# Kernel optimization log

Hardware: AMD Instinct MI355X
Metric: run time of the kernel (lower is better)

The kernel has to match this reference:

```python
import jax, jax.numpy as jnp
import numpy as np

B, T, DIM = 4, 2048, 2048
H = 16
Q_LORA, KV_LORA = 1536, 512
ROPE_D, NOPE_D, V_D = 64, 128, 128
Q_HEAD_D = NOPE_D + ROPE_D  # 192
EPS = 1e-6
ROPE_THETA = 500000.0


def rmsnorm(x, w):
    xf = x.astype(jnp.float32)
    rms = jax.lax.rsqrt(jnp.mean(xf * xf, axis=-1, keepdims=True) + EPS)
    return (xf * rms).astype(x.dtype) * w


def apply_rope(x, cos, sin):
    # x: (B,T,H,d); cos/sin: (T,d//2). Complex mult on interleaved pairs.
    d = x.shape[-1]
    xp = x.reshape(*x.shape[:-1], d // 2, 2)
    x0, x1 = xp[..., 0], xp[..., 1]
    c = cos[None, :, None, :]
    s = sin[None, :, None, :]
    o0 = x0 * c - x1 * s
    o1 = x0 * s + x1 * c
    return jnp.stack([o0, o1], axis=-1).reshape(x.shape)


def setup_inputs() -> dict:
    key = jax.random.key(0)
    ks = jax.random.split(key, 8)
    x = jax.random.normal(ks[0], (B, T, DIM), dtype=jnp.float32)
    # RoPE freqs as in standard precompute_freqs_cis
    inv_freq = 1.0 / (ROPE_THETA ** (np.arange(0, ROPE_D, 2, dtype=np.float32) / ROPE_D))
    t = np.arange(T, dtype=np.float32)
    ang = np.outer(t, inv_freq)  # (T, 32)
    freqs_cos = jnp.asarray(np.cos(ang))
    freqs_sin = jnp.asarray(np.sin(ang))
    # causal additive mask (1,1,T,T)
    mask = jnp.where(jnp.tril(jnp.ones((T, T), dtype=bool)), 0.0, -1e9).astype(jnp.float32)[None, None]
    sc = lambda fan_in: 1.0 / np.sqrt(fan_in)
    q_down_w = jax.random.normal(ks[1], (Q_LORA, DIM), dtype=jnp.float32) * sc(DIM)
    q_norm_w = jnp.ones((Q_LORA,), dtype=jnp.float32)
    q_up_nope_w = jax.random.normal(ks[2], (H * NOPE_D, Q_LORA), dtype=jnp.float32) * sc(Q_LORA)
    q_up_rope_w = jax.random.normal(ks[3], (H * ROPE_D, Q_LORA), dtype=jnp.float32) * sc(Q_LORA)
    kv_down_w = jax.random.normal(ks[4], (KV_LORA + ROPE_D, DIM), dtype=jnp.float32) * sc(DIM)
    kv_norm_w = jnp.ones((KV_LORA,), dtype=jnp.float32)
    kv_up_w = jax.random.normal(ks[5], (H * (NOPE_D + V_D), KV_LORA), dtype=jnp.float32) * sc(KV_LORA)
    wo_w = jax.random.normal(ks[6], (DIM, H * V_D), dtype=jnp.float32) * sc(H * V_D)
    return {"x": x, "freqs_cos": freqs_cos, "freqs_sin": freqs_sin, "mask": mask,
            "q_down_w": q_down_w, "q_norm_w": q_norm_w, "q_up_nope_w": q_up_nope_w,
            "q_up_rope_w": q_up_rope_w, "kv_down_w": kv_down_w, "kv_norm_w": kv_norm_w,
            "kv_up_w": kv_up_w, "wo_w": wo_w}


def reference(x, freqs_cos, freqs_sin, mask, q_down_w, q_norm_w, q_up_nope_w,
              q_up_rope_w, kv_down_w, kv_norm_w, kv_up_w, wo_w):
    b, t, _ = x.shape
    # Q path: low-rank down -> RMSNorm -> nope/rope up projections
    c_q = rmsnorm(x @ q_down_w.T, q_norm_w)                      # (B,T,q_lora)
    q_nope = (c_q @ q_up_nope_w.T).reshape(b, t, H, NOPE_D)
    q_rope = (c_q @ q_up_rope_w.T).reshape(b, t, H, ROPE_D)
    q_rope = apply_rope(q_rope, freqs_cos, freqs_sin)
    q = jnp.concatenate([q_nope, q_rope], axis=-1)               # (B,T,H,192)
    # KV path: shared low-rank latent + per-sequence rope key
    kv_raw = x @ kv_down_w.T                                     # (B,T,512+64)
    c_kv = kv_raw[..., :KV_LORA]
    k_rope = kv_raw[..., KV_LORA:][:, :, None, :]                # (B,T,1,64)
    k_rope = apply_rope(k_rope, freqs_cos, freqs_sin)
    k_rope = jnp.broadcast_to(k_rope, (b, t, H, ROPE_D))
    kv = (rmsnorm(c_kv, kv_norm_w) @ kv_up_w.T).reshape(b, t, H, NOPE_D + V_D)
    k_nope = kv[..., :NOPE_D]
    v = kv[..., NOPE_D:]                                         # (B,T,H,128)
    k = jnp.concatenate([k_nope, k_rope], axis=-1)               # (B,T,H,192)
    scale = Q_HEAD_D ** -0.5
    attn = jnp.einsum('bthd,bshd->bhts', q, k) * scale + mask    # (B,H,T,T)
    attn = jax.nn.softmax(attn, axis=-1)
    out = jnp.einsum('bhts,bshd->bthd', attn, v).reshape(b, t, H * V_D)
    return out @ wo_w.T
```

## Files before the change

kernel.cpp:

```cpp
#include <hip/hip_runtime.h>

#define BB 4
#define TT 2048
#define HH 16
#define ROWS (BB*TT)

typedef unsigned short u16;
typedef __bf16 bf16x8 __attribute__((ext_vector_type(8)));
typedef float f32x4 __attribute__((ext_vector_type(4)));
typedef u16 u16x8 __attribute__((ext_vector_type(8)));
typedef u16 u16x4 __attribute__((ext_vector_type(4)));

__device__ __forceinline__ u16 f2bf(float f) {
  unsigned u = __float_as_uint(f);
  u += 0x7fffu + ((u >> 16) & 1u);
  return (u16)(u >> 16);
}
__device__ __forceinline__ float bf2f(u16 h) {
  return __uint_as_float(((unsigned)h) << 16);
}

__device__ __forceinline__ void gload_lds16(const u16* g, u16* l) {
  __builtin_amdgcn_global_load_lds((const __attribute__((address_space(1))) void*)g,
                                   (__attribute__((address_space(3))) void*)l, 16, 0, 0);
}

__global__ __launch_bounds__(256) void cast_all(const float* __restrict__ x,
                                                const float* __restrict__ qdw,
                                                const float* __restrict__ kvdw,
                                                const float* __restrict__ qunw,
                                                const float* __restrict__ qurw,
                                                const float* __restrict__ kvuw,
                                                const float* __restrict__ wow,
                                                u16* __restrict__ xb,
                                                u16* __restrict__ wdc,
                                                u16* __restrict__ wuc,
                                                u16* __restrict__ wkvu,
                                                u16* __restrict__ wwo,
                                                float qsc) {
  const long s0 = 1536L*2048, s1 = 768L*2048, s2 = 2048L*1536,
             s3 = 1024L*1536, s4 = 4096L*512,  s5 = 2048L*2048,
             s6 = (long)ROWS*2048;
  const long total = s0+s1+s2+s3+s4+s5+s6;
  long i = ((long)blockIdx.x * 256 + threadIdx.x) * 4;
  long stride = (long)gridDim.x * 1024;
  for (; i < total; i += stride) {
    long off = i; const float* src; u16* dst; float sc = 1.f; long lim = -1;
    if (off < s0)               { src = qdw;  dst = wdc; }
    else if ((off -= s0) < s1)  { src = kvdw; dst = wdc + s0; lim = 576L*2048; }
    else if ((off -= s1) < s2)  { src = qunw; dst = wuc; sc = qsc; }
    else if ((off -= s2) < s3)  { src = qurw; dst = wuc + s2; }
    else if ((off -= s3) < s4)  { src = kvuw; dst = wkvu; }
    else if ((off -= s4) < s5)  { src = wow;  dst = wwo; }
    else { off -= s5;             src = x;    dst = xb; }
    u16x4 o;
    if (lim < 0 || off + 3 < lim) {
      float4 v = *(const float4*)(src + off);
      o = (u16x4){ f2bf(v.x*sc), f2bf(v.y*sc), f2bf(v.z*sc), f2bf(v.w*sc) };
    } else {
#pragma unroll
      for (int e = 0; e < 4; ++e) o[e] = (off + e < lim) ? f2bf(src[off+e]*sc) : (u16)0;
    }
    *(u16x4*)(dst + off) = o;
  }
}

template<int MODE>
__global__ __launch_bounds__(512, 2) void gemm256(const u16* __restrict__ A,
                                                  const u16* __restrict__ Bm,
                                                  void* __restrict__ Cv,
                                                  u16* __restrict__ Vt,
                                                  int M, int N, int K, int lda) {
  __shared__ __align__(16) u16 lds[32768];
  const int tid = threadIdx.x;
  const int lane = tid & 63, wid = tid >> 6;
  const int wm = (wid >> 2) * 128;
  const int wn = (wid & 3) * 64;

  const int nx = gridDim.x;
  int id = blockIdx.y * nx + blockIdx.x;
  const int cpx = (nx * gridDim.y) >> 3;
  id = (id & 7) * cpx + (id >> 3);
  const int m0 = (id / nx) * 256;
  const int n0 = (id % nx) * 256;

  const int NT = K >> 5;

  f32x4 acc[8][4] = {};

  auto stage = [&](int kt, int d) {
#pragma unroll
    for (int j = 0; j < 2; ++j) {
      int c = j*512 + tid;
      int row = c >> 2;
      int colb = (c & 3) << 4;
      int srcb = colb ^ (((row >> 1) & 3) << 4);
      const u16* ga = (const u16*)((const char*)A + ((long)(m0 + row) * lda + kt*32) * 2 + srcb);
      gload_lds16(ga, (u16*)((char*)lds + d*32768 + c*16));
      const u16* gb = (const u16*)((const char*)Bm + ((long)(n0 + row) * K + kt*32) * 2 + srcb);
      gload_lds16(gb, (u16*)((char*)lds + d*32768 + 16384 + c*16));
    }
  };

  stage(0, 0);
  stage(1, 1);

  const int lr = lane & 15;
  const int kb = (lane >> 4) << 4;

  for (int kt = 0; kt < NT; ++kt) {
    const int cur = kt & 1;
    if (kt + 1 < NT) asm volatile("s_waitcnt vmcnt(4)" ::: "memory");
    else             asm volatile("s_waitcnt vmcnt(0)" ::: "memory");
    __builtin_amdgcn_s_barrier();
    __builtin_amdgcn_sched_barrier(0);

    const char* Ab = (const char*)lds + cur*32768;
    const char* Bb = Ab + 16384;
    bf16x8 af[8], bf[4];
#pragma unroll
    for (int i = 0; i < 8; ++i) {
      int r = wm + i*16 + lr;
      af[i] = *(const bf16x8*)(Ab + r*64 + (kb ^ (((r >> 1) & 3) << 4)));
    }
#pragma unroll
    for (int i = 0; i < 4; ++i) {
      int r = wn + i*16 + lr;
      bf[i] = *(const bf16x8*)(Bb + r*64 + (kb ^ (((r >> 1) & 3) << 4)));
    }
    __builtin_amdgcn_s_setprio(1);
#pragma unroll
    for (int i = 0; i < 8; ++i)
#pragma unroll
      for (int j = 0; j < 4; ++j)
        acc[i][j] = __builtin_amdgcn_mfma_f32_16x16x32_bf16(af[i], bf[j], acc[i][j], 0, 0, 0);
    __builtin_amdgcn_s_setprio(0);
    __builtin_amdgcn_sched_barrier(0);
    __builtin_amdgcn_s_barrier();
    if (kt + 2 < NT) stage(kt + 2, cur);
  }

  const int orow = (lane >> 4) << 2;
  const int ocol = lane & 15;
#pragma unroll
  for (int mf = 0; mf < 8; ++mf)
#pragma unroll
    for (int nf = 0; nf < 4; ++nf) {
      long rbase = (long)(m0 + wm + mf*16 + orow);
      int col = n0 + wn + nf*16 + ocol;
      if (MODE == 0) {
#pragma unroll
        for (int rr = 0; rr < 4; ++rr)
          ((float*)Cv)[(rbase + rr) * (long)N + col] = acc[mf][nf][rr];
      } else if (MODE == 1) {
#pragma unroll
        for (int rr = 0; rr < 4; ++rr)
          ((u16*)Cv)[(rbase + rr) * (long)N + col] = f2bf(acc[mf][nf][rr]);
      } else {
        int h = col >> 8, inner = col & 255;
        if (inner < 128) {
#pragma unroll
          for (int rr = 0; rr < 4; ++rr)
            ((u16*)Cv)[(rbase + rr) * 2048L + h*128 + inner] = f2bf(acc[mf][nf][rr]);
        } else {
          int bb = (int)(rbase >> 11);
          int t  = (int)(rbase & 2047);
          long vo = ((long)(bb*16 + h) * 128 + (inner - 128)) * 2048 + t;
          u16x4 o = { f2bf(acc[mf][nf][0]), f2bf(acc[mf][nf][1]),
                      f2bf(acc[mf][nf][2]), f2bf(acc[mf][nf][3]) };
          *(u16x4*)(Vt + vo) = o;
        }
      }
    }
}

__global__ __launch_bounds__(256) void rms_rope_dk(u16* __restrict__ dk,
                                                   const float* __restrict__ qnw,
                                                   const float* __restrict__ kvnw,
                                                   u16* __restrict__ Kr,
                                                   const float* __restrict__ cosb,
                                                   const float* __restrict__ sinb) {
  const long row = blockIdx.x;
  u16* x = dk + row * 2304;
  const int i = threadIdx.x * 8;
  float sq = 0.f, sk = 0.f;
  u16x8 v = *(const u16x8*)(x + i);
  {
    float s = 0.f;
#pragma unroll
    for (int e = 0; e < 8; ++e) { float f = bf2f(v[e]); s += f*f; }
    if (i < 1536) sq = s; else sk = s;
  }
#pragma unroll
  for (int off = 32; off > 0; off >>= 1) {
    sq += __shfl_down(sq, off);
    sk += __shfl_down(sk, off);
  }
  __shared__ float redq[4], redk[4];
  if ((threadIdx.x & 63) == 0) {
    redq[threadIdx.x >> 6] = sq;
    redk[threadIdx.x >> 6] = sk;
  }
  __syncthreads();
  float rq = rsqrtf((redq[0]+redq[1]+redq[2]+redq[3]) * (1.f/1536.f) + 1e-6f);
  float rk = rsqrtf((redk[0]+redk[1]+redk[2]+redk[3]) * (1.f/512.f) + 1e-6f);
  {
    float r = (i < 1536) ? rq : rk;
    const float* w = (i < 1536) ? (qnw + i) : (kvnw + (i - 1536));
    u16x8 o;
#pragma unroll
    for (int e = 0; e < 8; ++e) o[e] = f2bf(bf2f(v[e]) * r * w[e]);
    *(u16x8*)(x + i) = o;
  }
  if (threadIdx.x < 32) {
    const int t = (int)(row & (TT-1));
    int ii = threadIdx.x;
    float x0 = bf2f(x[2048 + 2*ii]);
    float x1 = bf2f(x[2048 + 2*ii + 1]);
    float c = cosb[t*32 + ii], s = sinb[t*32 + ii];
    Kr[row*64 + 2*ii]     = f2bf(x0*c - x1*s);
    Kr[row*64 + 2*ii + 1] = f2bf(x0*s + x1*c);
  }
}

__global__ __launch_bounds__(512) void flash_attn10(const u16* __restrict__ qcat,
                                                    const u16* __restrict__ kn,
                                                    const u16* __restrict__ kr,
                                                    const u16* __restrict__ Vt,
                                                    const float* __restrict__ cosb,
                                                    const float* __restrict__ sinb,
                                                    u16* __restrict__ O) {
  __shared__ __align__(16) u16 lds[36864];
  const int bid = blockIdx.x;
  const int u = bid & 255, sl = bid >> 8;
  const int a = u >> 6;
  const int bh = u & 63;
  const int qt = sl ? a : (7 - a);
  const int b = bh >> 4, h = bh & 15;
  const int wid = threadIdx.x >> 6, lane = threadIdx.x & 63;
  const int q0 = qt*256 + wid*32;
  const long browq = (long)b * TT + q0;
  const long browk = (long)b * TT;
  const int l16 = lane >> 4;
  const int l8  = lane >> 3;
  const int lx16   = (lane & 15) * 16;
  const int lx8_16 = (lane & 7) * 16;
  const int co = l16 * 16;
  const float QSCE = 0.10411754661f;

  bf16x8 qf[2][6];
#pragma unroll
  for (int f = 0; f < 2; ++f) {
    long row = browq + f*16 + (lane & 15);
#pragma unroll
    for (int ks = 0; ks < 4; ++ks)
      qf[f][ks] = *(const bf16x8*)(qcat + row * 3072 + h*128 + ks*32 + l16 * 8);
    const int t = (int)(row & (TT-1));
#pragma unroll
    for (int ks = 0; ks < 2; ++ks) {
      bf16x8 v = *(const bf16x8*)(qcat + row * 3072 + 2048 + h*64 + ks*32 + l16 * 8);
      const int ib = ks*16 + l16*4;
#pragma unroll
      for (int pp = 0; pp < 4; ++pp) {
        float x0 = (float)v[2*pp], x1 = (float)v[2*pp+1];
        float c = cosb[t*32 + ib + pp], s = sinb[t*32 + ib + pp];
        v[2*pp]   = (__bf16)((x0*c - x1*s) * QSCE);
        v[2*pp+1] = (__bf16)((x0*s + x1*c) * QSCE);
      }
      qf[f][4+ks] = v;
    }
  }

  bf16x8 vones;
#pragma unroll
  for (int e = 0; e < 8; ++e) vones[e] = (__bf16)1.0f;

  f32x4 oacc[2][8] = {};
  f32x4 lsum[2] = {};

  u16* pw = lds + 20480 + wid * 2048;

  const int nIter = 4*qt + 4;
  for (int it = 0; it < nIter; ++it) {
    const int s0 = it * 64;
#pragma unroll
    for (int j = 0; j < 2; ++j) {
      int c = j*8 + wid;
      int r = c*4 + l16;
      int cb = lx16 ^ ((r & 7) << 4);
      const u16* src = (const u16*)((const char*)kn + (browk + s0 + r) * 4096 + h * 256 + cb);
      gload_lds16(src, lds + c*512);
    }
    {
      int c = wid;
      int r = c*8 + l8;
      int cb = lx8_16 ^ ((r & 7) << 4);
      const u16* src = (const u16*)((const char*)kr + (browk + s0 + r) * 128 + cb);
      gload_lds16(src, lds + 8192 + c*512);
    }
#pragma unroll
    for (int j = 0; j < 2; ++j) {
      int c = j*8 + wid;
      int d = c*8 + l8;
      int cb = lx8_16 ^ ((d & 7) << 4);
      const u16* src = (const u16*)((const char*)Vt + ((long)bh*128 + d) * (TT*2) + (long)s0*2 + cb);
      gload_lds16(src, lds + 12288 + c*512);
    }
    __syncthreads();

    const bool skip0 = s0 > q0 + 15;
    const bool skip1 = s0 > q0 + 31;
    if (!skip0 || !skip1) {
      __builtin_amdgcn_s_setprio(1);
      f32x4 sacc[2][4] = {};
#pragma unroll
      for (int nt = 0; nt < 4; ++nt) {
        const int r = nt*16 + (lane & 15);
        const int swz = (r & 7) << 4;
        bf16x8 kf[6];
#pragma unroll
        for (int ks = 0; ks < 4; ++ks)
          kf[ks] = *(const bf16x8*)((const char*)lds + r*256 + ((ks*64 + co) ^ swz));
#pragma unroll
        for (int ks = 0; ks < 2; ++ks)
          kf[4+ks] = *(const bf16x8*)((const char*)lds + 16384 + r*128 + ((ks*64 + co) ^ swz));
        if (!skip0) {
#pragma unroll
          for (int ks = 0; ks < 6; ++ks)
            sacc[0][nt] = __builtin_amdgcn_mfma_f32_16x16x32_bf16(qf[0][ks], kf[ks], sacc[0][nt], 0, 0, 0);
        }
        if (!skip1) {
#pragma unroll
          for (int ks = 0; ks < 6; ++ks)
            sacc[1][nt] = __builtin_amdgcn_mfma_f32_16x16x32_bf16(qf[1][ks], kf[ks], sacc[1][nt], 0, 0, 0);
        }
      }
#pragma unroll
      for (int f = 0; f < 2; ++f) {
        const bool skipf = f ? skip1 : skip0;
        if (skipf) continue;
        const int qmin = q0 + f*16;
        const int qb = qmin + (l16 << 2);
        if (s0 + 63 > qmin) {
#pragma unroll
          for (int nt = 0; nt < 4; ++nt) {
            int sc = s0 + nt*16 + (lane & 15);
#pragma unroll
            for (int rr = 0; rr < 4; ++rr)
              if (sc > qb + rr) sacc[f][nt][rr] = -1e30f;
          }
        }
        const int lb2 = (lane & 15) * 2;
#pragma unroll
        for (int rr = 0; rr < 4; ++rr) {
          float p0 = exp2f(sacc[f][0][rr] - 16.f);
          float p1 = exp2f(sacc[f][1][rr] - 16.f);
          float p2 = exp2f(sacc[f][2][rr] - 16.f);
          float p3 = exp2f(sacc[f][3][rr] - 16.f);
          const int prow = f*16 + (l16 << 2) + rr;
          const int sw = (prow & 7) << 4;
          char* pb = (char*)pw + prow*128;
          *(u16*)(pb + ((     lb2) ^ sw)) = f2bf(p0);
          *(u16*)(pb + (( 32 + lb2) ^ sw)) = f2bf(p1);
          *(u16*)(pb + (( 64 + lb2) ^ sw)) = f2bf(p2);
          *(u16*)(pb + (( 96 + lb2) ^ sw)) = f2bf(p3);
        }
      }
#pragma unroll
      for (int ks = 0; ks < 2; ++ks) {
        const int cb = ks*64 + co;
        bf16x8 vf[8];
#pragma unroll
        for (int vt = 0; vt < 8; ++vt) {
          int row = vt*16 + (lane & 15);
          vf[vt] = *(const bf16x8*)((const char*)lds + 24576 + row*128 + (cb ^ ((row & 7) << 4)));
        }
#pragma unroll
        for (int f = 0; f < 2; ++f) {
          if (f ? skip1 : skip0) continue;
          int prow = f*16 + (lane & 15);
          bf16x8 pa = *(const bf16x8*)((const char*)pw + prow*128 + (cb ^ ((prow & 7) << 4)));
          lsum[f] = __builtin_amdgcn_mfma_f32_16x16x32_bf16(pa, vones, lsum[f], 0, 0, 0);
#pragma unroll
          for (int vt = 0; vt < 8; ++vt)
            oacc[f][vt] = __builtin_amdgcn_mfma_f32_16x16x32_bf16(pa, vf[vt], oacc[f][vt], 0, 0, 0);
        }
      }
      __builtin_amdgcn_s_setprio(0);
    }
    __syncthreads();
  }

#pragma unroll
  for (int f = 0; f < 2; ++f) {
    float inv[4];
#pragma unroll
    for (int rr = 0; rr < 4; ++rr) inv[rr] = 1.f / lsum[f][rr];
#pragma unroll
    for (int vt = 0; vt < 8; ++vt)
#pragma unroll
      for (int rr = 0; rr < 4; ++rr) {
        long row = browq + f*16 + (l16 << 2) + rr;
        int col = h*128 + vt*16 + (lane & 15);
        O[row * 2048 + col] = f2bf(oacc[f][vt][rr] * inv[rr]);
      }
  }
}

static inline long minl(long a, long b) { return a < b ? a : b; }

extern "C" void kernel_launch(void* const* d_in, const int* in_sizes, int n_in,
                              void* d_out, int out_size, void* d_ws, size_t ws_size,
                              hipStream_t stream) {
  const float* x    = (const float*)d_in[0];
  const float* fcos = (const float*)d_in[1];
  const float* fsin = (const float*)d_in[2];
  const float* qdw  = (const float*)d_in[4];
  const float* qnw  = (const float*)d_in[5];
  const float* qunw = (const float*)d_in[6];
  const float* qurw = (const float*)d_in[7];
  const float* kvdw = (const float*)d_in[8];
  const float* kvnw = (const float*)d_in[9];
  const float* kvuw = (const float*)d_in[10];
  const float* wow  = (const float*)d_in[11];
  float* out = (float*)d_out;

  char* p = (char*)d_ws;
  auto alloc = [&](size_t bytes) { char* r = p; p += (bytes + 255) & ~(size_t)255; return r; };

  u16* xb   = (u16*)alloc((size_t)ROWS*2048*2);
  u16* wdc  = (u16*)alloc((size_t)2304*2048*2);
  u16* wuc  = (u16*)alloc((size_t)3072*1536*2);
  u16* wkvu = (u16*)alloc((size_t)4096*512*2);
  u16* wwo  = (u16*)alloc((size_t)2048*2048*2);
  u16* dk   = (u16*)alloc((size_t)ROWS*2304*2);
  u16* qcat = (u16*)alloc((size_t)ROWS*3072*2);
  u16* kn   = (u16*)alloc((size_t)ROWS*2048*2);
  u16* Vt   = (u16*)alloc((size_t)ROWS*2048*2);
  u16* kro  = (u16*)alloc((size_t)ROWS*64*2);

  u16* Ob = xb;

  const float QSC_E = 0.10411754661f;

  cast_all<<<4096, 256, 0, stream>>>(x, qdw, kvdw, qunw, qurw, kvuw, wow,
                                     xb, wdc, wuc, wkvu, wwo, QSC_E);

  gemm256<1><<<dim3(9, 32), 512, 0, stream>>>(xb, wdc, dk, nullptr, ROWS, 2304, 2048, 2048);
  rms_rope_dk<<<ROWS, 256, 0, stream>>>(dk, qnw, kvnw, kro, fcos, fsin);
  gemm256<1><<<dim3(12, 32), 512, 0, stream>>>(dk, wuc, qcat, nullptr, ROWS, 3072, 1536, 2304);
  gemm256<2><<<dim3(16, 32), 512, 0, stream>>>(dk + 1536, wkvu, kn, Vt, ROWS, 4096, 512, 2304);
  flash_attn10<<<512, 512, 0, stream>>>(qcat, kn, kro, Vt, fcos, fsin, Ob);
  gemm256<0><<<dim3(8, 32), 512, 0, stream>>>(Ob, wwo, out, nullptr, ROWS, 2048, 2048, 2048);
}
```

Before: 538.6 us.

## Add split-K-half pipelined GEMM variant for kv_up and output projection

Introduces gemm256k, a 256x256 tile GEMM that stages each 64-wide K tile as two 32-wide halves in double-buffered LDS. It issues next-tile loads interleaved between MFMA groups, using partial vmcnt waits and s_setprio around the MFMAs. It also remaps block IDs into 8 groups to improve L2 locality. The kv_up and wo GEMMs switch to this kernel, aiming to overlap global-to-LDS traffic with compute; the finer-grained barriers add synchronization cost.

```diff
diff --git a/kernel.cpp b/kernel.cpp
--- a/kernel.cpp
+++ b/kernel.cpp
@@ -174,6 +174,125 @@
     }
 }
 
+template<int MODE>
+__global__ __launch_bounds__(512, 2) void gemm256k(const u16* __restrict__ A,
+                                                   const u16* __restrict__ Bm,
+                                                   void* __restrict__ Cv,
+                                                   u16* __restrict__ Vt,
+                                                   int M, int N, int K, int lda) {
+  __shared__ __align__(16) u16 lds[65536];
+  const int tid = threadIdx.x;
+  const int lane = tid & 63, wid = tid >> 6;
+  const int wm = (wid >> 2) * 128;
+  const int wn = (wid & 3) * 64;
+
+  const int nx = gridDim.x;
+  int id = blockIdx.y * nx + blockIdx.x;
+  const int cpx = (nx * gridDim.y) >> 3;
+  id = (id & 7) * cpx + (id >> 3);
+  const int m0 = (id / nx) * 256;
+  const int n0 = (id % nx) * 256;
+
+  const int NT = K >> 6;
+
+  f32x4 acc[8][4] = {};
+
+  auto stageH = [&](int mat, int j, int t) {
+    const int d = t & 1;
+    char* base = (char*)lds + mat*65536 + (j*2 + d)*16384;
+    const u16* G = mat ? Bm : A;
+    const int r0 = mat ? n0 : m0;
+    const long ld = mat ? (long)K : (long)lda;
+#pragma unroll
+    for (int j2 = 0; j2 < 2; ++j2) {
+      int c = j2*512 + tid;
+      int row = c >> 2;
+      int colb = (c & 3) << 4;
+      int srcb = colb ^ (((row >> 1) & 3) << 4);
+      const u16* g = (const u16*)((const char*)G + ((long)(r0 + row) * ld + t*64 + j*32) * 2 + srcb);
+      gload_lds16(g, (u16*)(base + c*16));
+    }
+  };
+
+  stageH(0, 0, 0); stageH(1, 0, 0); stageH(0, 1, 0); stageH(1, 1, 0);
+
+  const int lr = lane & 15;
+  const int kb = (lane >> 4) << 4;
+
+  for (int t = 0; t < NT; ++t) {
+    const int d = t & 1;
+#pragma unroll
+    for (int half = 0; half < 2; ++half) {
+      if (half == 0 || t + 1 < NT) asm volatile("s_waitcnt vmcnt(4)" ::: "memory");
+      else                         asm volatile("s_waitcnt vmcnt(0)" ::: "memory");
+      __builtin_amdgcn_s_barrier();
+      __builtin_amdgcn_sched_barrier(0);
+
+      const char* Ab = (const char*)lds + (half*2 + d)*16384;
+      const char* Bb = (const char*)lds + 65536 + (half*2 + d)*16384;
+      bf16x8 bf[4];
+#pragma unroll
+      for (int nb = 0; nb < 4; ++nb) {
+        int r = wn + nb*16 + lr;
+        bf[nb] = *(const bf16x8*)(Bb + r*64 + (kb ^ (((r >> 1) & 3) << 4)));
+      }
+#pragma unroll
+      for (int c = 0; c < 2; ++c) {
+        bf16x8 af[4];
+#pragma unroll
+        for (int i = 0; i < 4; ++i) {
+          int r = wm + c*64 + i*16 + lr;
+          af[i] = *(const bf16x8*)(Ab + r*64 + (kb ^ (((r >> 1) & 3) << 4)));
+        }
+        if (t + 1 < NT) {
+          int pidx = half*2 + c;
+          stageH(pidx & 1, pidx >> 1, t + 1);
+        }
+        __builtin_amdgcn_s_setprio(1);
+#pragma unroll
+        for (int i = 0; i < 4; ++i)
+#pragma unroll
+          for (int nb = 0; nb < 4; ++nb)
+            acc[c*4 + i][nb] = __builtin_amdgcn_mfma_f32_16x16x32_bf16(af[i], bf[nb], acc[c*4+i][nb], 0, 0, 0);
+        __builtin_amdgcn_s_setprio(0);
+      }
+    }
+  }
+
+  const int orow = (lane >> 4) << 2;
+  const int ocol = lane & 15;
+#pragma unroll
+  for (int mf = 0; mf < 8; ++mf)
+#pragma unroll
+    for (int nf = 0; nf < 4; ++nf) {
+      long rbase = (long)(m0 + wm + mf*16 + orow);
+      int col = n0 + wn + nf*16 + ocol;
+      if (MODE == 0) {
+#pragma unroll
+        for (int rr = 0; rr < 4; ++rr)
+          ((float*)Cv)[(rbase + rr) * (long)N + col] = acc[mf][nf][rr];
+      } else if (MODE == 1) {
+#pragma unroll
+        for (int rr = 0; rr < 4; ++rr)
+          ((u16*)Cv)[(rbase + rr) * (long)N + col] = f2bf(acc[mf][nf][rr]);
+      } else {
+        int h = col >> 8, inner = col & 255;
+        if (inner < 128) {
+#pragma unroll
+          for (int rr = 0; rr < 4; ++rr)
+            ((u16*)Cv)[(rbase + rr) * 2048L + h*128 + inner] = f2bf(acc[mf][nf][rr]);
+        } else {
+          int bb = (int)(rbase >> 11);
+          int t2 = (int)(rbase & 2047);
+          long vo = ((long)(bb*16 + h) * 128 + (inner - 128)) * 2048 + t2;
+          u16x4 o = { f2bf(acc[mf][nf][0]), f2bf(acc[mf][nf][1]),
+                      f2bf(acc[mf][nf][2]), f2bf(acc[mf][nf][3]) };
+          *(u16x4*)(Vt + vo) = o;
+        }
+      }
+    }
+}
+
 __global__ __launch_bounds__(256) void rms_rope_dk(u16* __restrict__ dk,
                                                    const float* __restrict__ qnw,
                                                    const float* __restrict__ kvnw,
@@ -449,7 +568,7 @@
   gemm256<1><<<dim3(9, 32), 512, 0, stream>>>(xb, wdc, dk, nullptr, ROWS, 2304, 2048, 2048);
   rms_rope_dk<<<ROWS, 256, 0, stream>>>(dk, qnw, kvnw, kro, fcos, fsin);
   gemm256<1><<<dim3(12, 32), 512, 0, stream>>>(dk, wuc, qcat, nullptr, ROWS, 3072, 1536, 2304);
-  gemm256<2><<<dim3(16, 32), 512, 0, stream>>>(dk + 1536, wkvu, kn, Vt, ROWS, 4096, 512, 2304);
+  gemm256k<2><<<dim3(16, 32), 512, 0, stream>>>(dk + 1536, wkvu, kn, Vt, ROWS, 4096, 512, 2304);
   flash_attn10<<<512, 512, 0, stream>>>(qcat, kn, kro, Vt, fcos, fsin, Ob);
-  gemm256<0><<<dim3(8, 32), 512, 0, stream>>>(Ob, wwo, out, nullptr, ROWS, 2048, 2048, 2048);
-}
+  gemm256k<0><<<dim3(8, 32), 512, 0, stream>>>(Ob, wwo, out, nullptr, ROWS, 2048, 2048, 2048);
+}
```

New measurement: 575.9 us. +6.9%, slower.
